# Optimization experiments

Hardware: AMD Instinct MI355X
Metric: run time of the kernel (lower is better)

The kernel has to match this reference:

```python
import jax, jax.numpy as jnp
import numpy as np

B, NOP, NMA = 16, 512, 64
D_OP, D_MA, D_EG = 16, 8, 8
HID, OUT = 256, 128
NEG_SLOPE = 0.2


def _mlp(x, w1, b1, w2, b2, w3, b3):
    # Linear -> ELU -> Linear -> ELU -> Linear (MLPs.project)
    h = jax.nn.elu(x @ w1 + b1)
    h = jax.nn.elu(h @ w2 + b2)
    return h @ w3 + b3


def _gatop(op, ma, eg, ma_adj, pre_adj, sub_adj, attn_pre, params):
    # params: list of 5 tuples (w1,b1,w2,b2,w3,b3) for gnn_layers[0..4]
    num = op.shape[1]
    # flag_ma=0 aggregation: adj[...,None]*op[:,None,:,:] summed over dim -2 == adj @ op
    pre_f1 = _mlp(jnp.einsum('bij,bjd->bid', pre_adj, op), *params[1])   # [B,NOP,OUT]
    sub_f1 = _mlp(jnp.einsum('bij,bjd->bid', sub_adj, op), *params[2])   # [B,NOP,OUT]
    self_f1 = _mlp(op, *params[3])  # identity adjacency -> aggregation is op itself
    # machine-edge features: [B,NOP,NMA,D_MA+D_EG]
    ma_eg = jnp.concatenate([ma_adj[..., None] * ma[:, None, :, :], eg], axis=-1)
    # flag_ma=1: mask then per-pair MLP -> [B,NOP,NMA,OUT]
    ma_f1 = _mlp(ma_adj[..., None] * ma_eg, *params[0])
    # flag_ma=2: mean over machines counting nonzero entries
    cnt = jnp.sum(ma_f1 != 0.0, axis=-2).astype(ma_f1.dtype)
    ma_f2 = _mlp(jnp.sum(ma_f1, axis=-2) / cnt, *params[4])              # [B,NOP,OUT]
    # NOTE: original code uses attn_pre for ALL four scores (faithful)
    att = lambda f: jnp.sum(f * attn_pre, axis=-1, keepdims=True)        # [B,NOP,1]
    pre_ut, sub_ut, self_ut, ma_ut = att(pre_f1), att(sub_f1), att(self_f1), att(ma_f2)
    lrelu = lambda x: jax.nn.leaky_relu(x, NEG_SLOPE)
    scores = jnp.concatenate([
        lrelu(pre_ut + self_ut), lrelu(sub_ut + self_ut),
        lrelu(self_ut + self_ut), lrelu(ma_ut + self_ut)], axis=1)       # [B,4*NOP,1]
    alpha = jax.nn.softmax(scores, axis=1)
    a_pre = alpha[:, :num]
    a_sub = alpha[:, num:2 * num]
    a_self = alpha[:, 2 * num:3 * num]
    a_ma = alpha[:, 3 * num:]
    return jax.nn.sigmoid(a_pre * pre_f1 + a_sub * sub_f1 + a_self * self_f1 + a_ma * ma_f2)


def setup_inputs() -> dict:
    key = jax.random.key(0)
    ks = jax.random.split(key, 40)
    inp = {
        'op': jax.random.normal(ks[0], (B, NOP, D_OP), jnp.float32),
        'ma': jax.random.normal(ks[1], (B, NMA, D_MA), jnp.float32),
        'eg': jax.random.normal(ks[2], (B, NOP, NMA, D_EG), jnp.float32),
        'op_ma_adj': jax.random.randint(ks[3], (B, NOP, NMA), 0, 2, jnp.int32),
        'op_pre_adj': jax.random.randint(ks[4], (B, NOP, NOP), 0, 2, jnp.int32),
        'op_sub_adj': jax.random.randint(ks[5], (B, NOP, NOP), 0, 2, jnp.int32),
        'batch_idxes': jnp.arange(B, dtype=jnp.int32),
        'attn_pre': jax.random.normal(ks[6], (1, 1, OUT), jnp.float32) * 0.1,
    }
    ins = [D_MA + D_EG, D_OP, D_OP, D_OP, OUT]
    k = 7
    for i, din in enumerate(ins):
        inp[f'm{i}_w1'] = jax.random.normal(ks[k], (din, HID), jnp.float32) / np.sqrt(din); k += 1
        inp[f'm{i}_b1'] = jnp.zeros((HID,), jnp.float32)
        inp[f'm{i}_w2'] = jax.random.normal(ks[k], (HID, HID), jnp.float32) / np.sqrt(HID); k += 1
        inp[f'm{i}_b2'] = jnp.zeros((HID,), jnp.float32)
        inp[f'm{i}_w3'] = jax.random.normal(ks[k], (HID, OUT), jnp.float32) / np.sqrt(HID); k += 1
        inp[f'm{i}_b3'] = jnp.zeros((OUT,), jnp.float32)
    return inp


def reference(op, ma, eg, op_ma_adj, op_pre_adj, op_sub_adj, batch_idxes, attn_pre,
              m0_w1, m0_b1, m0_w2, m0_b2, m0_w3, m0_b3,
              m1_w1, m1_b1, m1_w2, m1_b2, m1_w3, m1_b3,
              m2_w1, m2_b1, m2_w2, m2_b2, m2_w3, m2_b3,
              m3_w1, m3_b1, m3_w2, m3_b2, m3_w3, m3_b3,
              m4_w1, m4_b1, m4_w2, m4_b2, m4_w3, m4_b3):
    ma_adj = op_ma_adj[batch_idxes].astype(op.dtype)
    pre_adj = op_pre_adj[batch_idxes].astype(op.dtype)
    sub_adj = op_sub_adj[batch_idxes].astype(op.dtype)
    params = [
        (m0_w1, m0_b1, m0_w2, m0_b2, m0_w3, m0_b3),
        (m1_w1, m1_b1, m1_w2, m1_b2, m1_w3, m1_b3),
        (m2_w1, m2_b1, m2_w2, m2_b2, m2_w3, m2_b3),
        (m3_w1, m3_b1, m3_w2, m3_b2, m3_w3, m3_b3),
        (m4_w1, m4_b1, m4_w2, m4_b2, m4_w3, m4_b3),
    ]
    return _gatop(op, ma, eg, ma_adj, pre_adj, sub_adj, attn_pre, params)
```

## Files before the change

### kernel.cpp

```cpp
#include <hip/hip_runtime.h>
#include <math.h>

#define NBb  16
#define NOPc 512
#define NMAc 64
#define HIDc 256
#define OUTc 128
#define NROW (NBb * NOPc)
#define NEMAX (NROW * NMAc)

#define HX(row, col) ((col) ^ (8 * ((row) & 15)))
#define FX(row, col) ((col) ^ (4 * ((row) & 15)))

typedef unsigned int uint32;
typedef unsigned short ush;
typedef __attribute__((ext_vector_type(8))) short bf16x8;
typedef __attribute__((ext_vector_type(4))) float f32x4;

__device__ __forceinline__ ush f2bf(float v) {
    uint32 u = __float_as_uint(v);
    u += 0x7FFFu + ((u >> 16) & 1u);
    return (ush)(u >> 16);
}
__device__ __forceinline__ float bf2f(ush b) { return __uint_as_float(((uint32)b) << 16); }
__device__ __forceinline__ float eluf(float x) { return x > 0.f ? x : expm1f(x); }
__device__ __forceinline__ float eluf_fast(float x) { return x > 0.f ? x : __expf(x) - 1.f; }
__device__ __forceinline__ uint32 pkbf(float a, float b) {
    return __builtin_amdgcn_perm(__float_as_uint(b), __float_as_uint(a), 0x07060302u);
}
__device__ __forceinline__ uint32 pkbf_rne(float a, float b) {
    return (uint32)f2bf(a) | ((uint32)f2bf(b) << 16);
}
__device__ __forceinline__ void split2(float a, float b, uint32& hp, uint32& lp) {
    const uint32 ua = __float_as_uint(a), ub = __float_as_uint(b);
    hp = __builtin_amdgcn_perm(ub, ua, 0x07060302u);
    const float ra = a - __uint_as_float(ua & 0xFFFF0000u);
    const float rb = b - __uint_as_float(ub & 0xFFFF0000u);
    lp = __builtin_amdgcn_perm(__float_as_uint(rb), __float_as_uint(ra), 0x07060302u);
}

#define MFMA(A, B, C) __builtin_amdgcn_mfma_f32_16x16x32_bf16((A), (B), (C), 0, 0, 0)

struct MlpPack {
    const ush *w1h, *w1l, *w2h, *w2l, *w3h, *w3l;
    const float *b1, *b2, *b3;
};

__device__ __forceinline__ void mlp3_core32(
    const MlpPack& P, const int KB1,
    const ush* Xh, const ush* Xl, ush* Hh, ush* Hl, f32x4 acc3[2][2])
{
    const int tid = threadIdx.x;
    const int wv = tid >> 6, lane = tid & 63, r = lane & 15, g = lane >> 4;
    const int KX = KB1 * 32;

    {
        f32x4 acc[4][2];
        #pragma unroll
        for (int a = 0; a < 4; ++a) {
            const float4 bv = *(const float4*)(P.b1 + (wv * 4 + a) * 16 + 4 * g);
            #pragma unroll
            for (int m = 0; m < 2; ++m) acc[a][m] = f32x4{bv.x, bv.y, bv.z, bv.w};
        }
        #pragma unroll 1
        for (int kb = 0; kb < KB1; ++kb) {
            bf16x8 wh[4], wl[4];
            #pragma unroll
            for (int a = 0; a < 4; ++a) {
                const size_t o = ((size_t)(kb * 16 + (wv * 4 + a)) * 64 + lane) * 8;
                wh[a] = *(const bf16x8*)(P.w1h + o);
                wl[a] = *(const bf16x8*)(P.w1l + o);
            }
            #pragma unroll
            for (int m = 0; m < 2; ++m) {
                const int row = 16 * m + r;
                const int ki = kb * 32 + 8 * g;
                bf16x8 xh = *(const bf16x8*)(Xh + row * KX + ki);
                bf16x8 xl = *(const bf16x8*)(Xl + row * KX + ki);
                #pragma unroll
                for (int a = 0; a < 4; ++a) {
                    acc[a][m] = MFMA(wh[a], xh, acc[a][m]);
                    acc[a][m] = MFMA(wh[a], xl, acc[a][m]);
                    acc[a][m] = MFMA(wl[a], xh, acc[a][m]);
                }
            }
        }
        #pragma unroll
        for (int a = 0; a < 4; ++a) {
            const int n0 = (wv * 4 + a) * 16 + 4 * g;
            #pragma unroll
            for (int m = 0; m < 2; ++m) {
                const int row = 16 * m + r;
                const float y0 = eluf_fast(acc[a][m][0]);
                const float y1 = eluf_fast(acc[a][m][1]);
                const float y2 = eluf_fast(acc[a][m][2]);
                const float y3 = eluf_fast(acc[a][m][3]);
                uint2 uh, ul;
                split2(y0, y1, uh.x, ul.x);
                split2(y2, y3, uh.y, ul.y);
                const int idx = row * 256 + HX(row, n0);
                *(uint2*)(Hh + idx) = uh;
                *(uint2*)(Hl + idx) = ul;
            }
        }
    }
    __syncthreads();

    {
        f32x4 acc[4][2];
        #pragma unroll
        for (int a = 0; a < 4; ++a) {
            const float4 bv = *(const float4*)(P.b2 + (wv * 4 + a) * 16 + 4 * g);
            #pragma unroll
            for (int m = 0; m < 2; ++m) acc[a][m] = f32x4{bv.x, bv.y, bv.z, bv.w};
        }
        #pragma unroll 1
        for (int kb = 0; kb < 8; ++kb) {
            bf16x8 wh[4], wl[4];
            #pragma unroll
            for (int a = 0; a < 4; ++a) {
                const size_t o = ((size_t)(kb * 16 + (wv * 4 + a)) * 64 + lane) * 8;
                wh[a] = *(const bf16x8*)(P.w2h + o);
                wl[a] = *(const bf16x8*)(P.w2l + o);
            }
            #pragma unroll
            for (int m = 0; m < 2; ++m) {
                const int row = 16 * m + r;
                const int k0 = kb * 32 + 8 * g;
                const int idx = row * 256 + HX(row, k0);
                bf16x8 hh = *(const bf16x8*)(Hh + idx);
                bf16x8 hl = *(const bf16x8*)(Hl + idx);
                #pragma unroll
                for (int a = 0; a < 4; ++a) {
                    acc[a][m] = MFMA(wh[a], hh, acc[a][m]);
                    acc[a][m] = MFMA(wh[a], hl, acc[a][m]);
                    acc[a][m] = MFMA(wl[a], hh, acc[a][m]);
                }
            }
        }
        __syncthreads();
        #pragma unroll
        for (int a = 0; a < 4; ++a) {
            const int n0 = (wv * 4 + a) * 16 + 4 * g;
            #pragma unroll
            for (int m = 0; m < 2; ++m) {
                const int row = 16 * m + r;
                const float y0 = eluf_fast(acc[a][m][0]);
                const float y1 = eluf_fast(acc[a][m][1]);
                const float y2 = eluf_fast(acc[a][m][2]);
                const float y3 = eluf_fast(acc[a][m][3]);
                uint2 uh, ul;
                split2(y0, y1, uh.x, ul.x);
                split2(y2, y3, uh.y, ul.y);
                const int idx = row * 256 + HX(row, n0);
                *(uint2*)(Hh + idx) = uh;
                *(uint2*)(Hl + idx) = ul;
            }
        }
    }
    __syncthreads();

    {
        #pragma unroll
        for (int a = 0; a < 2; ++a) {
            const float4 bv = *(const float4*)(P.b3 + (wv * 2 + a) * 16 + 4 * g);
            #pragma unroll
            for (int m = 0; m < 2; ++m) acc3[a][m] = f32x4{bv.x, bv.y, bv.z, bv.w};
        }
        #pragma unroll 1
        for (int kb = 0; kb < 8; ++kb) {
            bf16x8 wh[2], wl[2];
            #pragma unroll
            for (int a = 0; a < 2; ++a) {
                const size_t o = ((size_t)(kb * 8 + (wv * 2 + a)) * 64 + lane) * 8;
                wh[a] = *(const bf16x8*)(P.w3h + o);
                wl[a] = *(const bf16x8*)(P.w3l + o);
            }
            #pragma unroll
            for (int m = 0; m < 2; ++m) {
                const int row = 16 * m + r;
                const int k0 = kb * 32 + 8 * g;
                const int idx = row * 256 + HX(row, k0);
                bf16x8 hh = *(const bf16x8*)(Hh + idx);
                bf16x8 hl = *(const bf16x8*)(Hl + idx);
                #pragma unroll
                for (int a = 0; a < 2; ++a) {
                    acc3[a][m] = MFMA(wh[a], hh, acc3[a][m]);
                    acc3[a][m] = MFMA(wh[a], hl, acc3[a][m]);
                    acc3[a][m] = MFMA(wl[a], hh, acc3[a][m]);
                }
            }
        }
    }
}

__global__ __launch_bounds__(256) void count_kernel(const int* __restrict__ ma_adj,
                                                    const int* __restrict__ bidx,
                                                    int* __restrict__ counts)
{
    const int tid = threadIdx.x;
    const int rid = blockIdx.x * 4 + (tid >> 6);
    const int lane = tid & 63;
    const int b = rid >> 9, i = rid & 511;
    const int bi = bidx[b];
    const int active = (ma_adj[((size_t)bi * NOPc + i) * NMAc + lane] != 0) ? 1 : 0;
    const unsigned long long mk = __ballot(active);
    if (lane == 0) counts[rid] = (int)__popcll(mk);
}

__global__ __launch_bounds__(1024) void scan_kernel(const int* __restrict__ counts,
                                                    int* __restrict__ bases,
                                                    int* __restrict__ natot,
                                                    ush* __restrict__ Xq,
                                                    ush* __restrict__ rowseg)
{
    __shared__ int tot[1024];
    const int t = threadIdx.x;
    int loc[8];
    int s = 0;
    #pragma unroll
    for (int k = 0; k < 8; ++k) { loc[k] = s; s += counts[t * 8 + k]; }
    tot[t] = s;
    __syncthreads();
    for (int off = 1; off < 1024; off <<= 1) {
        const int v = (t >= off) ? tot[t - off] : 0;
        __syncthreads();
        tot[t] += v;
        __syncthreads();
    }
    const int base = tot[t] - s;
    #pragma unroll
    for (int k = 0; k < 8; ++k) bases[t * 8 + k] = base + loc[k];
    const int NA = tot[1023];
    if (t == 0) *natot = NA;
    __syncthreads();
    const int NApad = (NA + 63) & ~63;
    for (int idx = NA * 16 + t; idx < NApad * 16; idx += 1024) Xq[idx] = 0;
    for (int idx = NA + t; idx < NApad; idx += 1024) rowseg[idx] = (ush)0xFFFFu;
}

struct PackDesc { const float* src; ush* dh; ush* dl; int kreal; int kbn; int nbn; };
struct PrepArgs {
    PackDesc d[15];
    const float* op; const int* pre_adj; const int* sub_adj; const int* ma_adj;
    const int* bidx;
    float* pre_agg; float* sub_agg;
    const float *z_b1, *z_w2, *z_b2, *z_w3, *z_b3;
    float* f1z;
    const float* ma; const float* eg; const int* bases;
    ush* Xq; ush* rowseg; float* sumG;
};

__global__ __launch_bounds__(256) void prep_kernel(PrepArgs A)
{
    __shared__ float shmem[9216];
    const int blk = blockIdx.x;
    const int t = threadIdx.x;
    if (blk < 960) {
        const PackDesc d = A.d[blk >> 6];
        const int sub = blk & 63;
        const int total = d.kbn * d.nbn * 512;
        const int N = d.nbn * 16;
        for (int idx = sub * 256 + t; idx < total; idx += 64 * 256) {
            const int e = idx & 7;
            const int l = (idx >> 3) & 63;
            const int t2 = idx >> 9;
            const int nb = t2 % d.nbn;
            const int kb = t2 / d.nbn;
            const int k = kb * 32 + ((l >> 4) << 3) + e;
            const int n = nb * 16 + (l & 15);
            const float v = (k < d.kreal) ? d.src[(size_t)k * N + n] : 0.f;
            const ush hi = f2bf(v);
            d.dh[idx] = hi;
            d.dl[idx] = f2bf(v - bf2f(hi));
        }
    } else if (blk < 1984) {
        const int e = blk - 960;
        const int b = e >> 6;
        const int i0 = (e & 63) * 8;
        const int bi = A.bidx[b];
        float* opS = shmem;
        float* red = shmem + 8704;
        {
            const float4* op4 = (const float4*)(A.op + (size_t)b * 8192);
            for (int idx4 = t; idx4 < 2048; idx4 += 256) {
                const float4 v = op4[idx4];
                const int row = idx4 >> 2, d0 = (idx4 & 3) * 4;
                float* dst = &opS[row * 17 + d0];
                dst[0] = v.x; dst[1] = v.y; dst[2] = v.z; dst[3] = v.w;
            }
        }
        __syncthreads();
        const int d = t & 15, g = t >> 4;
        for (int ii = 0; ii < 8; ++ii) {
            const int i = i0 + ii;
            const int4* pr4 = (const int4*)(A.pre_adj + ((size_t)bi * NOPc + i) * NOPc);
            const int4* sr4 = (const int4*)(A.sub_adj + ((size_t)bi * NOPc + i) * NOPc);
            float ap = 0.f, as = 0.f;
            #pragma unroll 2
            for (int j4 = g; j4 < 128; j4 += 16) {
                const int4 p = pr4[j4];
                const int4 s = sr4[j4];
                const int jb = j4 << 2;
                const float v0 = opS[(jb + 0) * 17 + d];
                const float v1 = opS[(jb + 1) * 17 + d];
                const float v2 = opS[(jb + 2) * 17 + d];
                const float v3 = opS[(jb + 3) * 17 + d];
                if (p.x) ap += v0;  if (p.y) ap += v1;  if (p.z) ap += v2;  if (p.w) ap += v3;
                if (s.x) as += v0;  if (s.y) as += v1;  if (s.z) as += v2;  if (s.w) as += v3;
            }
            red[g * 16 + d] = ap;
            red[256 + g * 16 + d] = as;
            __syncthreads();
            if (t < 32) {
                const int which = t >> 4, dd = t & 15;
                float s = 0.f;
                #pragma unroll
                for (int gg = 0; gg < 16; ++gg) s += red[which * 256 + gg * 16 + dd];
                float* dst = which ? A.sub_agg : A.pre_agg;
                dst[((size_t)b * NOPc + i) * 16 + dd] = s;
            }
            __syncthreads();
        }
    } else if (blk == 1984) {
        shmem[t] = eluf(A.z_b1[t]);
        __syncthreads();
        float acc = A.z_b2[t];
        for (int k = 0; k < 256; ++k) acc += shmem[k] * A.z_w2[(size_t)k * 256 + t];
        __syncthreads();
        shmem[256 + t] = eluf(acc);
        __syncthreads();
        if (t < 128) {
            float a = A.z_b3[t];
            for (int k = 0; k < 256; ++k) a += shmem[256 + k] * A.z_w3[(size_t)k * 128 + t];
            A.f1z[t] = a;
        }
    } else {
        const int rid = (blk - 1985) * 4 + (t >> 6);
        const int lane = t & 63;
        const int b = rid >> 9, i = rid & 511;
        const int bi = A.bidx[b];
        const int act = (A.ma_adj[((size_t)bi * NOPc + i) * NMAc + lane] != 0) ? 1 : 0;
        const unsigned long long mk = __ballot(act);
        if (act) {
            const int pos = A.bases[rid] + (int)__popcll(mk & ((1ull << lane) - 1ull));
            const float4* mp = (const float4*)(A.ma + ((size_t)b * NMAc + lane) * 8);
            const float4* ep = (const float4*)(A.eg + (((size_t)b * NOPc + i) * NMAc + lane) * 8);
            const float4 m0 = mp[0], m1 = mp[1], e0 = ep[0], e1 = ep[1];
            uint4 u0, u1;
            u0.x = pkbf_rne(m0.x, m0.y); u0.y = pkbf_rne(m0.z, m0.w);
            u0.z = pkbf_rne(m1.x, m1.y); u0.w = pkbf_rne(m1.z, m1.w);
            u1.x = pkbf_rne(e0.x, e0.y); u1.y = pkbf_rne(e0.z, e0.w);
            u1.z = pkbf_rne(e1.x, e1.y); u1.w = pkbf_rne(e1.z, e1.w);
            uint4* dst = (uint4*)(A.Xq + (size_t)pos * 16);
            dst[0] = u0;
            dst[1] = u1;
            A.rowseg[pos] = (ush)rid;
        }
        A.sumG[(size_t)rid * 128 + lane] = 0.f;
        A.sumG[(size_t)rid * 128 + 64 + lane] = 0.f;
    }
}

struct EF1Args {
    const ush* Xq; const ush* rowseg; const int* natot; MlpPack P0;
    float* sumG;
    const float* X[3]; MlpPack P[3]; float* f1[3]; float* ut[3];
};

__global__ __launch_bounds__(256, 4) void edge_f1_kernel(EF1Args A, const float* __restrict__ attn)
{
    __shared__ unsigned char smem[36992];
    const int blk = blockIdx.x;
    const int tid = threadIdx.x;
    const int wv = tid >> 6, lane = tid & 63, r = lane & 15, g = lane >> 4;

    if (blk < 8192) {
        const int NA = *A.natot;
        const int tile = blk;
        if (tile * 64 >= NA) return;
        ush* Hh = (ush*)smem;
        ush* segid = (ush*)(smem + 32768);
        const MlpPack& P = A.P0;
        if (tid < 64) segid[tid] = A.rowseg[(size_t)tile * 64 + tid];

        {
            f32x4 acc[4][4];
            #pragma unroll
            for (int a = 0; a < 4; ++a) {
                const float4 bv = *(const float4*)(P.b1 + (wv * 4 + a) * 16 + 4 * g);
                #pragma unroll
                for (int m = 0; m < 4; ++m) acc[a][m] = f32x4{bv.x, bv.y, bv.z, bv.w};
            }
            bf16x8 wh[4];
            #pragma unroll
            for (int a = 0; a < 4; ++a)
                wh[a] = *(const bf16x8*)(P.w1h + ((size_t)(wv * 4 + a) * 64 + lane) * 8);
            #pragma unroll
            for (int m = 0; m < 4; ++m) {
                const int gr = tile * 64 + 16 * m + r;
                bf16x8 xh = {0, 0, 0, 0, 0, 0, 0, 0};
                if (g < 2) xh = *(const bf16x8*)(A.Xq + (size_t)gr * 16 + 8 * g);
                #pragma unroll
                for (int a = 0; a < 4; ++a) acc[a][m] = MFMA(wh[a], xh, acc[a][m]);
            }
            #pragma unroll
            for (int a = 0; a < 4; ++a) {
                const int n0 = (wv * 4 + a) * 16 + 4 * g;
                #pragma unroll
                for (int m = 0; m < 4; ++m) {
                    const int row = 16 * m + r;
                    const float y0 = eluf_fast(acc[a][m][0]);
                    const float y1 = eluf_fast(acc[a][m][1]);
                    const float y2 = eluf_fast(acc[a][m][2]);
                    const float y3 = eluf_fast(acc[a][m][3]);
                    uint2 u; u.x = pkbf(y0, y1); u.y = pkbf(y2, y3);
                    *(uint2*)(Hh + row * 256 + HX(row, n0)) = u;
                }
            }
        }
        __syncthreads();

        {
            f32x4 acc[4][4];
            #pragma unroll
            for (int a = 0; a < 4; ++a) {
                const float4 bv = *(const float4*)(P.b2 + (wv * 4 + a) * 16 + 4 * g);
                #pragma unroll
                for (int m = 0; m < 4; ++m) acc[a][m] = f32x4{bv.x, bv.y, bv.z, bv.w};
            }
            #pragma unroll 1
            for (int kb = 0; kb < 8; ++kb) {
                bf16x8 wh[4];
                #pragma unroll
                for (int a = 0; a < 4; ++a)
                    wh[a] = *(const bf16x8*)(P.w2h + ((size_t)(kb * 16 + (wv * 4 + a)) * 64 + lane) * 8);
                #pragma unroll
                for (int m = 0; m < 4; ++m) {
                    const int row = 16 * m + r;
                    const int k0 = kb * 32 + 8 * g;
                    bf16x8 hh = *(const bf16x8*)(Hh + row * 256 + HX(row, k0));
                    #pragma unroll
                    for (int a = 0; a < 4; ++a) acc[a][m] = MFMA(wh[a], hh, acc[a][m]);
                }
            }
            __syncthreads();
            #pragma unroll
            for (int a = 0; a < 4; ++a) {
                const int n0 = (wv * 4 + a) * 16 + 4 * g;
                #pragma unroll
                for (int m = 0; m < 4; ++m) {
                    const int row = 16 * m + r;
                    const float y0 = eluf_fast(acc[a][m][0]);
                    const float y1 = eluf_fast(acc[a][m][1]);
                    const float y2 = eluf_fast(acc[a][m][2]);
                    const float y3 = eluf_fast(acc[a][m][3]);
                    uint2 u; u.x = pkbf(y0, y1); u.y = pkbf(y2, y3);
                    *(uint2*)(Hh + row * 256 + HX(row, n0)) = u;
                }
            }
        }
        __syncthreads();

        f32x4 acc3[2][4];
        #pragma unroll
        for (int a = 0; a < 2; ++a) {
            const float4 bv = *(const float4*)(P.b3 + (wv * 2 + a) * 16 + 4 * g);
            #pragma unroll
            for (int m = 0; m < 4; ++m) acc3[a][m] = f32x4{bv.x, bv.y, bv.z, bv.w};
        }
        #pragma unroll 1
        for (int kb = 0; kb < 8; ++kb) {
            bf16x8 wh[2];
            #pragma unroll
            for (int a = 0; a < 2; ++a)
                wh[a] = *(const bf16x8*)(P.w3h + ((size_t)(kb * 8 + (wv * 2 + a)) * 64 + lane) * 8);
            #pragma unroll
            for (int m = 0; m < 4; ++m) {
                const int row = 16 * m + r;
                const int k0 = kb * 32 + 8 * g;
                bf16x8 hh = *(const bf16x8*)(Hh + row * 256 + HX(row, k0));
                #pragma unroll
                for (int a = 0; a < 2; ++a) acc3[a][m] = MFMA(wh[a], hh, acc3[a][m]);
            }
        }
        __syncthreads();

        float* f1buf = (float*)Hh;
        #pragma unroll
        for (int a = 0; a < 2; ++a) {
            const int n0 = (wv * 2 + a) * 16 + 4 * g;
            #pragma unroll
            for (int m = 0; m < 4; ++m) {
                const int row = 16 * m + r;
                float4 y;
                y.x = acc3[a][m][0];
                y.y = acc3[a][m][1];
                y.z = acc3[a][m][2];
                y.w = acc3[a][m][3];
                *(float4*)&f1buf[row * 128 + FX(row, n0)] = y;
            }
        }
        __syncthreads();

        {
            const int c = tid & 127, h = tid >> 7;
            const int r0p = h * 32;
            float accS = 0.f;
            int cur = -1;
            #pragma unroll
            for (int j = 0; j < 32; ++j) {
                const int rl = r0p + j;
                const int sg = (int)segid[rl];
                if (sg != cur) {
                    if ((unsigned)cur < (unsigned)NROW)
                        atomicAdd(&A.sumG[(size_t)cur * 128 + c], accS);
                    cur = sg; accS = 0.f;
                }
                accS += f1buf[rl * 128 + FX(rl, c)];
            }
            if ((unsigned)cur < (unsigned)NROW)
                atomicAdd(&A.sumG[(size_t)cur * 128 + c], accS);
        }
    } else {
        const int pb = blk - 8192;
        const int p = pb >> 8;
        const int row0 = (pb & 255) * 32;
        ush* Xh = (ush*)smem;
        ush* Xl = (ush*)(smem + 2048);
        ush* Hh = (ush*)(smem + 4096);
        ush* Hl = (ush*)(smem + 20480);
        float* UT = (float*)(smem + 36864);
        const float* Xg = A.X[p];
        const MlpPack P = A.P[p];
        float* f1_out = A.f1[p];
        float* ut_out = A.ut[p];
        if (tid < 32) UT[tid] = 0.f;
        for (int idx = tid; idx < 32 * 32; idx += 256) {
            const int row = idx >> 5, k = idx & 31;
            float v = 0.f;
            if (k < 16) v = Xg[(size_t)(row0 + row) * 16 + k];
            const uint32 uv = __float_as_uint(v);
            Xh[idx] = (ush)(uv >> 16);
            const float rest = v - __uint_as_float(uv & 0xFFFF0000u);
            Xl[idx] = (ush)(__float_as_uint(rest) >> 16);
        }
        __syncthreads();
        f32x4 acc3[2][2];
        mlp3_core32(P, 1, Xh, Xl, Hh, Hl, acc3);

        float utp[2] = {0.f, 0.f};
        #pragma unroll
        for (int a = 0; a < 2; ++a) {
            const int n0 = (wv * 2 + a) * 16 + 4 * g;
            const float4 av = *(const float4*)(attn + n0);
            #pragma unroll
            for (int m = 0; m < 2; ++m) {
                float4 y;
                y.x = acc3[a][m][0];
                y.y = acc3[a][m][1];
                y.z = acc3[a][m][2];
                y.w = acc3[a][m][3];
                *(float4*)&f1_out[(size_t)(row0 + 16 * m + r) * OUTc + n0] = y;
                utp[m] += y.x * av.x + y.y * av.y + y.z * av.z + y.w * av.w;
            }
        }
        #pragma unroll
        for (int m = 0; m < 2; ++m) {
            float v = utp[m];
            v += __shfl_xor(v, 16);
            v += __shfl_xor(v, 32);
            if (lane < 16) atomicAdd(&UT[16 * m + r], v);
        }
        __syncthreads();
        if (tid < 32) ut_out[row0 + tid] = UT[tid];
    }
}

__global__ __launch_bounds__(256, 3) void p3_kernel(
    MlpPack P, const float* __restrict__ attn,
    const float* __restrict__ sumG,
    const int* __restrict__ counts, const float* __restrict__ f1z,
    float* __restrict__ f1_out, float* __restrict__ ut_out)
{
    __shared__ ush Xh[32 * 128], Xl[32 * 128];
    __shared__ ush Hh[32 * 256], Hl[32 * 256];
    __shared__ float UT[32];
    const int tid = threadIdx.x;
    const int row0 = blockIdx.x * 32;
    if (tid < 32) UT[tid] = 0.f;
    for (int idx = tid; idx < 32 * 128; idx += 256) {
        const int row = idx >> 7, k = idx & 127;
        const size_t rid = (size_t)(row0 + row);
        const float na = (float)counts[rid];
        const float nz = 64.f - na;
        const float fz = f1z[k];
        const float v = (sumG[rid * 128 + k] + nz * fz)
                      / (na + nz * ((fz != 0.f) ? 1.f : 0.f));
        const uint32 uv = __float_as_uint(v);
        Xh[idx] = (ush)(uv >> 16);
        const float rest = v - __uint_as_float(uv & 0xFFFF0000u);
        Xl[idx] = (ush)(__float_as_uint(rest) >> 16);
    }
    __syncthreads();
    f32x4 acc3[2][2];
    mlp3_core32(P, 4, Xh, Xl, Hh, Hl, acc3);

    const int wv = tid >> 6, lane = tid & 63, r = lane & 15, g = lane >> 4;
    float utp[2] = {0.f, 0.f};
    #pragma unroll
    for (int a = 0; a < 2; ++a) {
        const int n0 = (wv * 2 + a) * 16 + 4 * g;
        const float4 av = *(const float4*)(attn + n0);
        #pragma unroll
        for (int m = 0; m < 2; ++m) {
            float4 y;
            y.x = acc3[a][m][0];
            y.y = acc3[a][m][1];
            y.z = acc3[a][m][2];
            y.w = acc3[a][m][3];
            *(float4*)&f1_out[(size_t)(row0 + 16 * m + r) * OUTc + n0] = y;
            utp[m] += y.x * av.x + y.y * av.y + y.z * av.z + y.w * av.w;
        }
    }
    #pragma unroll
    for (int m = 0; m < 2; ++m) {
        float v = utp[m];
        v += __shfl_xor(v, 16);
        v += __shfl_xor(v, 32);
        if (lane < 16) atomicAdd(&UT[16 * m + r], v);
    }
    __syncthreads();
    if (tid < 32) ut_out[row0 + tid] = UT[tid];
}

__global__ __launch_bounds__(256) void combine2_kernel(
    const float* __restrict__ uts,
    const float* __restrict__ pre_f1, const float* __restrict__ sub_f1,
    const float* __restrict__ self_f1, const float* __restrict__ ma_f2,
    float* __restrict__ out)
{
    __shared__ float sc[4 * NOPc];
    __shared__ float red[256];
    const int b = blockIdx.x >> 4, chunk = blockIdx.x & 15;
    const int t = threadIdx.x;
    const float* put = uts + 0 * NROW + (size_t)b * NOPc;
    const float* sut = uts + 1 * NROW + (size_t)b * NOPc;
    const float* eut = uts + 2 * NROW + (size_t)b * NOPc;
    const float* mut = uts + 3 * NROW + (size_t)b * NOPc;
    for (int i = t; i < NOPc; i += 256) {
        const float se = eut[i];
        const float s0 = put[i] + se, s1 = sut[i] + se, s2 = se + se, s3 = mut[i] + se;
        sc[0 * NOPc + i] = s0 > 0.f ? s0 : 0.2f * s0;
        sc[1 * NOPc + i] = s1 > 0.f ? s1 : 0.2f * s1;
        sc[2 * NOPc + i] = s2 > 0.f ? s2 : 0.2f * s2;
        sc[3 * NOPc + i] = s3 > 0.f ? s3 : 0.2f * s3;
    }
    __syncthreads();
    float mx = -INFINITY;
    for (int idx = t; idx < 4 * NOPc; idx += 256) mx = fmaxf(mx, sc[idx]);
    red[t] = mx;
    __syncthreads();
    for (int s = 128; s > 0; s >>= 1) { if (t < s) red[t] = fmaxf(red[t], red[t + s]); __syncthreads(); }
    mx = red[0];
    __syncthreads();
    float ps = 0.f;
    for (int idx = t; idx < 4 * NOPc; idx += 256) {
        const float e = expf(sc[idx] - mx);
        sc[idx] = e;
        ps += e;
    }
    red[t] = ps;
    __syncthreads();
    for (int s = 128; s > 0; s >>= 1) { if (t < s) red[t] += red[t + s]; __syncthreads(); }
    const float invZ = 1.f / red[0];

    const size_t base4 = (size_t)b * 16384 + (size_t)chunk * 1024;
    #pragma unroll
    for (int k = 0; k < 4; ++k) {
        const size_t e4 = base4 + k * 256 + t;
        const int i = (int)((e4 >> 5) & 511);
        const float a0 = sc[0 * NOPc + i] * invZ;
        const float a1 = sc[1 * NOPc + i] * invZ;
        const float a2 = sc[2 * NOPc + i] * invZ;
        const float a3 = sc[3 * NOPc + i] * invZ;
        const float4 vp = ((const float4*)pre_f1)[e4];
        const float4 vs = ((const float4*)sub_f1)[e4];
        const float4 ve = ((const float4*)self_f1)[e4];
        const float4 vm = ((const float4*)ma_f2)[e4];
        float4 o;
        o.x = 1.f / (1.f + expf(-(a0 * vp.x + a1 * vs.x + a2 * ve.x + a3 * vm.x)));
        o.y = 1.f / (1.f + expf(-(a0 * vp.y + a1 * vs.y + a2 * ve.y + a3 * vm.y)));
        o.z = 1.f / (1.f + expf(-(a0 * vp.z + a1 * vs.z + a2 * ve.z + a3 * vm.z)));
        o.w = 1.f / (1.f + expf(-(a0 * vp.w + a1 * vs.w + a2 * ve.w + a3 * vm.w)));
        ((float4*)out)[e4] = o;
    }
}

extern "C" void kernel_launch(void* const* d_in, const int* in_sizes, int n_in,
                              void* d_out, int out_size, void* d_ws, size_t ws_size,
                              hipStream_t stream) {
    const float* op      = (const float*)d_in[0];
    const float* ma      = (const float*)d_in[1];
    const float* eg      = (const float*)d_in[2];
    const int*   ma_adj  = (const int*)d_in[3];
    const int*   pre_adj = (const int*)d_in[4];
    const int*   sub_adj = (const int*)d_in[5];
    const int*   bidx    = (const int*)d_in[6];
    const float* attn    = (const float*)d_in[7];
    float* out = (float*)d_out;
    const float* Wraw[5][6];
    for (int m = 0; m < 5; ++m)
        for (int j = 0; j < 6; ++j)
            Wraw[m][j] = (const float*)d_in[8 + 6 * m + j];

    float* wsf = (float*)d_ws;
    float* pre_agg = wsf;  wsf += (size_t)NROW * 16;
    float* sub_agg = wsf;  wsf += (size_t)NROW * 16;
    float* pre_f1  = wsf;  wsf += (size_t)NROW * OUTc;
    float* sub_f1  = wsf;  wsf += (size_t)NROW * OUTc;
    float* self_f1 = wsf;  wsf += (size_t)NROW * OUTc;
    float* ma_f2   = wsf;  wsf += (size_t)NROW * OUTc;
    float* uts     = wsf;  wsf += (size_t)4 * NROW;
    float* f1z     = wsf;  wsf += 128;
    float* sumG    = wsf;  wsf += (size_t)NROW * 128;
    int*   counts  = (int*)wsf;   wsf += NROW;
    int*   bases   = (int*)wsf;   wsf += NROW;
    int*   natot   = (int*)wsf;   wsf += 16;
    ush*   rowseg  = (ush*)wsf;   wsf += NEMAX / 2;
    ush*   Xq      = (ush*)wsf;   wsf += (size_t)NEMAX * 8;
    ush*   packp   = (ush*)wsf;

    PrepArgs pa;
    MlpPack pk[5];
    for (int m = 0; m < 5; ++m) {
        const int kre[3] = { (m == 4 ? 128 : 16), 256, 256 };
        const int kbn[3] = { (m == 4 ? 4 : 1), 8, 8 };
        const int nbn[3] = { 16, 16, 8 };
        const ush* dh[3]; const ush* dl[3];
        for (int j = 0; j < 3; ++j) {
            const int id = m * 3 + j;
            pa.d[id].src = Wraw[m][2 * j];
            pa.d[id].kreal = kre[j];
            pa.d[id].kbn = kbn[j];
            pa.d[id].nbn = nbn[j];
            const int cnt = kbn[j] * nbn[j] * 512;
            pa.d[id].dh = packp; dh[j] = packp; packp += cnt;
            pa.d[id].dl = packp; dl[j] = packp; packp += cnt;
        }
        pk[m].w1h = dh[0]; pk[m].w1l = dl[0];
        pk[m].w2h = dh[1]; pk[m].w2l = dl[1];
        pk[m].w3h = dh[2]; pk[m].w3l = dl[2];
        pk[m].b1 = Wraw[m][1]; pk[m].b2 = Wraw[m][3]; pk[m].b3 = Wraw[m][5];
    }
    pa.op = op; pa.pre_adj = pre_adj; pa.sub_adj = sub_adj; pa.ma_adj = ma_adj;
    pa.bidx = bidx;
    pa.pre_agg = pre_agg; pa.sub_agg = sub_agg;
    pa.z_b1 = Wraw[0][1]; pa.z_w2 = Wraw[0][2]; pa.z_b2 = Wraw[0][3];
    pa.z_w3 = Wraw[0][4]; pa.z_b3 = Wraw[0][5];
    pa.f1z = f1z;
    pa.ma = ma; pa.eg = eg; pa.bases = bases;
    pa.Xq = Xq; pa.rowseg = rowseg; pa.sumG = sumG;

    EF1Args ea;
    ea.Xq = Xq; ea.rowseg = rowseg; ea.natot = natot; ea.P0 = pk[0];
    ea.sumG = sumG;
    ea.X[0] = pre_agg; ea.X[1] = sub_agg; ea.X[2] = op;
    ea.P[0] = pk[1];   ea.P[1] = pk[2];   ea.P[2] = pk[3];
    ea.f1[0] = pre_f1; ea.f1[1] = sub_f1; ea.f1[2] = self_f1;
    ea.ut[0] = uts + 0 * NROW;
    ea.ut[1] = uts + 1 * NROW;
    ea.ut[2] = uts + 2 * NROW;

    count_kernel<<<dim3(NROW / 4), 256, 0, stream>>>(ma_adj, bidx, counts);
    scan_kernel<<<1, 1024, 0, stream>>>(counts, bases, natot, Xq, rowseg);
    prep_kernel<<<dim3(960 + 1024 + 1 + NROW / 4), 256, 0, stream>>>(pa);
    edge_f1_kernel<<<dim3(8192 + 768), 256, 0, stream>>>(ea, attn);
    p3_kernel<<<dim3(256), 256, 0, stream>>>(pk[4], attn, sumG, counts, f1z,
                                             ma_f2, uts + 3 * NROW);
    combine2_kernel<<<dim3(NBb * 16), 256, 0, stream>>>(uts, pre_f1, sub_f1, self_f1, ma_f2, out);
}
```

Measured before the change: 160.0 us.

## Compute pre/sub adjacency aggregation with bf16 MFMA using hi/lo split of op

Replaces the scalar masked-sum aggregation of pre_adj@op and sub_adj@op in prep_kernel with bf16 MFMA, converting the 0/1 adjacency to bf16 and splitting op into high and low bf16 parts for near-fp32 accuracy. Each block now handles 64 rows instead of 8, so far fewer blocks are launched and op is staged into LDS once per 64 rows rather than per 8. The per-row shared-memory reduction and its barriers go away. The trade-off is a slight precision change from the two-term bf16 split and less parallelism in this part of the kernel.

```diff
diff --git a/kernel.cpp b/kernel.cpp
--- a/kernel.cpp
+++ b/kernel.cpp
@@ -37,6 +37,9 @@
     const float ra = a - __uint_as_float(ua & 0xFFFF0000u);
     const float rb = b - __uint_as_float(ub & 0xFFFF0000u);
     lp = __builtin_amdgcn_perm(__float_as_uint(rb), __float_as_uint(ra), 0x07060302u);
+}
+__device__ __forceinline__ uint32 pkadj(int a, int b) {
+    return (a ? 0x3F80u : 0u) | (b ? 0x3F800000u : 0u);
 }
 
 #define MFMA(A, B, C) __builtin_amdgcn_mfma_f32_16x16x32_bf16((A), (B), (C), 0, 0, 0)
@@ -253,7 +256,7 @@
 
 __global__ __launch_bounds__(256) void prep_kernel(PrepArgs A)
 {
-    __shared__ float shmem[9216];
+    __shared__ float shmem[8192];
     const int blk = blockIdx.x;
     const int t = threadIdx.x;
     if (blk < 960) {
@@ -274,55 +277,60 @@
             d.dh[idx] = hi;
             d.dl[idx] = f2bf(v - bf2f(hi));
         }
-    } else if (blk < 1984) {
+    } else if (blk < 1088) {
         const int e = blk - 960;
-        const int b = e >> 6;
-        const int i0 = (e & 63) * 8;
+        const int b = e >> 3;
+        const int i0 = (e & 7) * 64;
         const int bi = A.bidx[b];
-        float* opS = shmem;
-        float* red = shmem + 8704;
-        {
-            const float4* op4 = (const float4*)(A.op + (size_t)b * 8192);
-            for (int idx4 = t; idx4 < 2048; idx4 += 256) {
-                const float4 v = op4[idx4];
-                const int row = idx4 >> 2, d0 = (idx4 & 3) * 4;
-                float* dst = &opS[row * 17 + d0];
-                dst[0] = v.x; dst[1] = v.y; dst[2] = v.z; dst[3] = v.w;
-            }
-        }
-        __syncthreads();
-        const int d = t & 15, g = t >> 4;
-        for (int ii = 0; ii < 8; ++ii) {
-            const int i = i0 + ii;
-            const int4* pr4 = (const int4*)(A.pre_adj + ((size_t)bi * NOPc + i) * NOPc);
-            const int4* sr4 = (const int4*)(A.sub_adj + ((size_t)bi * NOPc + i) * NOPc);
-            float ap = 0.f, as = 0.f;
-            #pragma unroll 2
-            for (int j4 = g; j4 < 128; j4 += 16) {
-                const int4 p = pr4[j4];
-                const int4 s = sr4[j4];
-                const int jb = j4 << 2;
-                const float v0 = opS[(jb + 0) * 17 + d];
-                const float v1 = opS[(jb + 1) * 17 + d];
-                const float v2 = opS[(jb + 2) * 17 + d];
-                const float v3 = opS[(jb + 3) * 17 + d];
-                if (p.x) ap += v0;  if (p.y) ap += v1;  if (p.z) ap += v2;  if (p.w) ap += v3;
-                if (s.x) as += v0;  if (s.y) as += v1;  if (s.z) as += v2;  if (s.w) as += v3;
-            }
-            red[g * 16 + d] = ap;
-            red[256 + g * 16 + d] = as;
-            __syncthreads();
-            if (t < 32) {
-                const int which = t >> 4, dd = t & 15;
-                float s = 0.f;
-                #pragma unroll
-                for (int gg = 0; gg < 16; ++gg) s += red[which * 256 + gg * 16 + dd];
-                float* dst = which ? A.sub_agg : A.pre_agg;
-                dst[((size_t)b * NOPc + i) * 16 + dd] = s;
-            }
-            __syncthreads();
-        }
-    } else if (blk == 1984) {
+        ush* opH = (ush*)shmem;
+        ush* opL = opH + 8192;
+        for (int idx = t; idx < 8192; idx += 256) {
+            const int j = idx >> 4, dd = idx & 15;
+            const float v = A.op[(size_t)b * 8192 + idx];
+            const int kb = j >> 5, gg = (j >> 3) & 3, ee = j & 7;
+            const int di = ((kb * 64 + gg * 16 + dd) << 3) + ee;
+            const uint32 uv = __float_as_uint(v);
+            opH[di] = (ush)(uv >> 16);
+            const float rest = v - __uint_as_float(uv & 0xFFFF0000u);
+            opL[di] = (ush)(__float_as_uint(rest) >> 16);
+        }
+        __syncthreads();
+        const int wv = t >> 6, lane = t & 63, r = lane & 15, g = lane >> 4;
+        const int i = i0 + wv * 16 + r;
+        const int4* pr4 = (const int4*)(A.pre_adj + ((size_t)bi * NOPc + i) * NOPc);
+        const int4* sr4 = (const int4*)(A.sub_adj + ((size_t)bi * NOPc + i) * NOPc);
+        f32x4 accP = {0.f, 0.f, 0.f, 0.f}, accS = {0.f, 0.f, 0.f, 0.f};
+        #pragma unroll 2
+        for (int kb = 0; kb < 16; ++kb) {
+            const int jo = kb * 8 + 2 * g;
+            const int4 p0 = pr4[jo], p1 = pr4[jo + 1];
+            const int4 s0 = sr4[jo], s1 = sr4[jo + 1];
+            bf16x8 ap, as;
+            {
+                uint32 u0 = pkadj(p0.x, p0.y), u1 = pkadj(p0.z, p0.w);
+                uint32 u2 = pkadj(p1.x, p1.y), u3 = pkadj(p1.z, p1.w);
+                uint32* pa = (uint32*)&ap;
+                pa[0] = u0; pa[1] = u1; pa[2] = u2; pa[3] = u3;
+            }
+            {
+                uint32 u0 = pkadj(s0.x, s0.y), u1 = pkadj(s0.z, s0.w);
+                uint32 u2 = pkadj(s1.x, s1.y), u3 = pkadj(s1.z, s1.w);
+                uint32* pa = (uint32*)&as;
+                pa[0] = u0; pa[1] = u1; pa[2] = u2; pa[3] = u3;
+            }
+            const bf16x8 oh = *(const bf16x8*)(opH + ((kb * 64 + lane) << 3));
+            const bf16x8 ol = *(const bf16x8*)(opL + ((kb * 64 + lane) << 3));
+            accP = MFMA(oh, ap, accP);
+            accP = MFMA(ol, ap, accP);
+            accS = MFMA(oh, as, accS);
+            accS = MFMA(ol, as, accS);
+        }
+        float4 vp, vs;
+        vp.x = accP[0]; vp.y = accP[1]; vp.z = accP[2]; vp.w = accP[3];
+        vs.x = accS[0]; vs.y = accS[1]; vs.z = accS[2]; vs.w = accS[3];
+        *(float4*)&A.pre_agg[((size_t)b * NOPc + i) * 16 + 4 * g] = vp;
+        *(float4*)&A.sub_agg[((size_t)b * NOPc + i) * 16 + 4 * g] = vs;
+    } else if (blk == 1088) {
         shmem[t] = eluf(A.z_b1[t]);
         __syncthreads();
         float acc = A.z_b2[t];
@@ -336,7 +344,7 @@
             A.f1z[t] = a;
         }
     } else {
-        const int rid = (blk - 1985) * 4 + (t >> 6);
+        const int rid = (blk - 1089) * 4 + (t >> 6);
         const int lane = t & 63;
         const int b = rid >> 9, i = rid & 511;
         const int bi = A.bidx[b];
@@ -774,7 +782,7 @@
 
     count_kernel<<<dim3(NROW / 4), 256, 0, stream>>>(ma_adj, bidx, counts);
     scan_kernel<<<1, 1024, 0, stream>>>(counts, bases, natot, Xq, rowseg);
-    prep_kernel<<<dim3(960 + 1024 + 1 + NROW / 4), 256, 0, stream>>>(pa);
+    prep_kernel<<<dim3(960 + 128 + 1 + NROW / 4), 256, 0, stream>>>(pa);
     edge_f1_kernel<<<dim3(8192 + 768), 256, 0, stream>>>(ea, attn);
     p3_kernel<<<dim3(256), 256, 0, stream>>>(pk[4], attn, sumG, counts, f1z,
                                              ma_f2, uts + 3 * NROW);
```

Result: faster. 147.7 us (-7.7%).
